# Performance work log

Hardware: AMD Instinct MI355X
Metric: run time of the kernel (lower is better)

## Reference

```python
import jax, jax.numpy as jnp
import numpy as np

EMB_DIM = 1024
NUM_HEAD = 16
HEAD_DIM = EMB_DIM // NUM_HEAD
B, S = 2, 2048


def setup_inputs() -> dict:
    key = jax.random.key(0)
    ks = jax.random.split(key, 10)
    scale = 1.0 / np.sqrt(EMB_DIM)
    x = jax.random.normal(ks[0], (B, S, EMB_DIM), dtype=jnp.float32)
    # causal mask: 1 = keep, 0 = masked out (torch masked_fill(mask == 0, -inf))
    mask = jnp.tril(jnp.ones((S, S), dtype=jnp.int32))[None, None, :, :]
    def lin(kw, kb):
        W = jax.random.uniform(kw, (EMB_DIM, EMB_DIM), jnp.float32, -scale, scale)
        b = jax.random.uniform(kb, (EMB_DIM,), jnp.float32, -scale, scale)
        return W, b
    Wq, bq = lin(ks[1], ks[2])
    Wk, bk = lin(ks[3], ks[4])
    Wv, bv = lin(ks[5], ks[6])
    Wo, bo = lin(ks[7], ks[8])
    return {"x": x, "mask": mask, "Wq": Wq, "bq": bq, "Wk": Wk, "bk": bk,
            "Wv": Wv, "bv": bv, "Wo": Wo, "bo": bo}


def reference(x, mask, Wq, bq, Wk, bk, Wv, bv, Wo, bo):
    Bsz, Sq, _ = x.shape
    # projections; torch Linear: y = x @ W^T + b
    def proj(W, b):
        y = jnp.einsum('bse,fe->bsf', x, W) + b
        return y.reshape(Bsz, Sq, NUM_HEAD, HEAD_DIM).transpose(0, 2, 1, 3)  # [B,H,S,D]
    q = proj(Wq, bq)
    k = proj(Wk, bk)
    v = proj(Wv, bv)
    scaling = jnp.asarray(HEAD_DIM ** 0.5, x.dtype)
    scores = jnp.einsum('bhqd,bhkd->bhqk', q, k) / scaling  # [B,H,S,S]
    scores = jnp.where(mask == 0, -jnp.inf, scores)
    attn = jax.nn.softmax(scores, axis=-1)
    out = jnp.einsum('bhqk,bhkd->bhqd', attn, v)
    out = out.transpose(0, 2, 1, 3).reshape(Bsz, Sq, EMB_DIM)
    return jnp.einsum('bse,fe->bsf', out, Wo) + bo
```

## Files before the change

kernel.cpp:

```cpp
#include <hip/hip_runtime.h>

typedef unsigned short u16;
typedef __attribute__((ext_vector_type(8))) __bf16 bf16x8;
typedef __attribute__((ext_vector_type(8))) short  short8;
typedef __attribute__((ext_vector_type(4))) short  short4v;
typedef __attribute__((ext_vector_type(4))) float  floatx4;

constexpr int Bc = 2, Sc = 2048, Ec = 1024, Hc = 16, Dc = 64;
constexpr int Mc = Bc * Sc;

#define NEG_BIG (-1.0e30f)

__device__ __forceinline__ u16 f2b(float f) {
  union { float f; unsigned u; } c; c.f = f;
  unsigned u = c.u;
  return (u16)((u + 0x7fffu + ((u >> 16) & 1u)) >> 16);
}
__device__ __forceinline__ short8 ld8(const u16* p) { return *(const short8*)p; }

__device__ __forceinline__ floatx4 mfma16(short8 a, short8 b, floatx4 c) {
  return __builtin_amdgcn_mfma_f32_16x16x32_bf16(
      __builtin_bit_cast(bf16x8, a), __builtin_bit_cast(bf16x8, b), c, 0, 0, 0);
}

__device__ __forceinline__ void async16(const u16* g, u16* l) {
  __builtin_amdgcn_global_load_lds(
      (const __attribute__((address_space(1))) void*)g,
      (__attribute__((address_space(3))) void*)l, 16, 0, 0);
}

__global__ __launch_bounds__(256) void cvt_kernel(
    const float* __restrict__ x,  const float* __restrict__ Wq,
    const float* __restrict__ Wk, const float* __restrict__ Wv,
    const float* __restrict__ Wo, u16* __restrict__ dst) {
  const size_t i = ((size_t)blockIdx.x * 256 + threadIdx.x) * 4;
  const int seg = (int)(i >> 20);
  const float* src;
  size_t off;
  if (seg < 4)       { src = x;  off = i; }
  else if (seg == 4) { src = Wq; off = i - ((size_t)4 << 20); }
  else if (seg == 5) { src = Wk; off = i - ((size_t)5 << 20); }
  else if (seg == 6) { src = Wv; off = i - ((size_t)6 << 20); }
  else               { src = Wo; off = i - ((size_t)7 << 20); }
  floatx4 v = *(const floatx4*)(src + off);
  short4v o;
  o[0] = (short)f2b(v[0]); o[1] = (short)f2b(v[1]);
  o[2] = (short)f2b(v[2]); o[3] = (short)f2b(v[3]);
  *(short4v*)(dst + i) = o;
}

__device__ __forceinline__ void gemm128(
    const u16* __restrict__ A, const u16* __restrict__ B, int K,
    int m0, int n0, u16* As, u16* Bs, floatx4 acc[4][4]) {
  const int t = threadIdx.x;
  const int w = t >> 6, lane = t & 63;
  const int wm = w & 1, wn = w >> 1;
  const int quad = lane >> 4, l16 = lane & 15;
  const int r = t >> 2;
  const int c = (t & 3) * 8;

#pragma unroll
  for (int i = 0; i < 4; ++i)
#pragma unroll
    for (int j = 0; j < 4; ++j) acc[i][j] = 0.f;

  for (int k0 = 0; k0 < K; k0 += 32) {
#pragma unroll
    for (int jj = 0; jj < 2; ++jj) {
      async16(A + (size_t)(m0 + jj * 64 + r) * K + k0 + c, As + jj * 2048 + w * 512);
      async16(B + (size_t)(n0 + jj * 64 + r) * K + k0 + c, Bs + jj * 2048 + w * 512);
    }
    __syncthreads();
    short8 af[4], bfr[4];
#pragma unroll
    for (int i = 0; i < 4; ++i)
      af[i]  = *(const short8*)(As + (wm * 64 + i * 16 + l16) * 32 + quad * 8);
#pragma unroll
    for (int j = 0; j < 4; ++j)
      bfr[j] = *(const short8*)(Bs + (wn * 64 + j * 16 + l16) * 32 + quad * 8);
#pragma unroll
    for (int i = 0; i < 4; ++i)
#pragma unroll
      for (int j = 0; j < 4; ++j)
        acc[i][j] = mfma16(af[i], bfr[j], acc[i][j]);
    __syncthreads();
  }
}

__global__ __launch_bounds__(256) void qkv_mm(
    const u16* __restrict__ xb, const u16* __restrict__ Wb,
    const float* __restrict__ bq, const float* __restrict__ bk,
    const float* __restrict__ bv,
    u16* __restrict__ Q, u16* __restrict__ K_, u16* __restrict__ Vt) {
  __shared__ __align__(16) u16 As[4096], Bs[4096];
  const int z = blockIdx.z;
  const u16* W = Wb + ((size_t)z << 20);
  const float* bias = (z == 0) ? bq : (z == 1) ? bk : bv;
  const int m0 = blockIdx.y * 128, n0 = blockIdx.x * 128;

  floatx4 acc[4][4];
  gemm128(xb, W, Ec, m0, n0, As, Bs, acc);

  const int t = threadIdx.x, w = t >> 6, lane = t & 63;
  const int wm = w & 1, wn = w >> 1, quad = lane >> 4, l16 = lane & 15;
#pragma unroll
  for (int i = 0; i < 4; ++i)
#pragma unroll
    for (int j = 0; j < 4; ++j)
#pragma unroll
      for (int rr = 0; rr < 4; ++rr) {
        const int row = m0 + wm * 64 + i * 16 + quad * 4 + rr;
        const int col = n0 + wn * 64 + j * 16 + l16;
        const float v = acc[i][j][rr] + bias[col];
        const int bb = row >> 11, s = row & (Sc - 1);
        const int h = col >> 6, d = col & (Dc - 1), bh = bb * Hc + h;
        if (z < 2) ((z == 0) ? Q : K_)[((size_t)bh * Sc + s) * Dc + d] = f2b(v);
        else       Vt[((size_t)bh * Dc + d) * Sc + s] = f2b(v);
      }
}

__global__ __launch_bounds__(256) void proj_mm(
    const u16* __restrict__ O, const u16* __restrict__ Wob,
    const float* __restrict__ bias, float* __restrict__ out) {
  __shared__ __align__(16) u16 As[4096], Bs[4096];
  const int m0 = blockIdx.y * 128, n0 = blockIdx.x * 128;

  floatx4 acc[4][4];
  gemm128(O, Wob, Ec, m0, n0, As, Bs, acc);

  const int t = threadIdx.x, w = t >> 6, lane = t & 63;
  const int wm = w & 1, wn = w >> 1, quad = lane >> 4, l16 = lane & 15;
#pragma unroll
  for (int i = 0; i < 4; ++i)
#pragma unroll
    for (int j = 0; j < 4; ++j)
#pragma unroll
      for (int rr = 0; rr < 4; ++rr) {
        const int row = m0 + wm * 64 + i * 16 + quad * 4 + rr;
        const int col = n0 + wn * 64 + j * 16 + l16;
        out[(size_t)row * Ec + col] = acc[i][j][rr] + bias[col];
      }
}

__device__ __forceinline__ void attn_stream(
    int q0, const u16* __restrict__ Qh, const u16* __restrict__ Kh,
    const u16* __restrict__ Vh, u16* __restrict__ O, int bb, int h,
    u16* Ks, u16* Vs, u16* Pw) {
  const int t = threadIdx.x;
  const int w = t >> 6, lane = t & 63;
  const int quad = lane >> 4, l16 = lane & 15;

  const int sr = w * 8 + (lane >> 3);
  const int sb = (lane & 7) ^ (lane >> 3);
  const int swz = l16 & 7;

  const u16* qrow_p = Qh + (size_t)(q0 + w * 16 + l16) * Dc;
  const short8 aq0 = ld8(qrow_p + quad * 8);
  const short8 aq1 = ld8(qrow_p + 32 + quad * 8);

  float   mrow[4], lrow[4];
  floatx4 oacc[4];
#pragma unroll
  for (int r = 0; r < 4; ++r) { mrow[r] = NEG_BIG; lrow[r] = 0.f; }
#pragma unroll
  for (int dt = 0; dt < 4; ++dt) oacc[dt] = 0.f;

  for (int kt = 0; kt <= q0; kt += 128) {
#pragma unroll
    for (int st = 0; st < 2; ++st)
#pragma unroll
      for (int it = 0; it < 2; ++it) {
        const int r = it * 32 + sr;
        async16(Kh + (size_t)(kt + st * 64 + r) * Dc + sb * 8,
                Ks + st * 4096 + it * 2048 + w * 512);
        async16(Vh + (size_t)r * Sc + kt + st * 64 + sb * 8,
                Vs + st * 4096 + it * 2048 + w * 512);
      }
    __syncthreads();

    floatx4 sacc[8];
#pragma unroll
    for (int nt = 0; nt < 8; ++nt) sacc[nt] = 0.f;
#pragma unroll
    for (int ks = 0; ks < 2; ++ks) {
      const short8 a = ks ? aq1 : aq0;
#pragma unroll
      for (int nt = 0; nt < 8; ++nt) {
        const short8 b = *(const short8*)(
            Ks + (nt >> 2) * 4096 + ((nt & 3) * 16 + l16) * 64 +
            (((ks * 4 + quad) ^ swz) * 8));
        sacc[nt] = mfma16(a, b, sacc[nt]);
      }
    }

    const bool diag = (kt + 128 > q0);
#pragma unroll
    for (int r = 0; r < 4; ++r) {
      const int qrow = q0 + w * 16 + quad * 4 + r;
      float sv[8];
      float mx = NEG_BIG;
#pragma unroll
      for (int nt = 0; nt < 8; ++nt) {
        float s = sacc[nt][r] * 0.125f;
        const int col = kt + nt * 16 + l16;
        s = (diag && col > qrow) ? NEG_BIG : s;
        sv[nt] = s;
        mx = fmaxf(mx, s);
      }
#pragma unroll
      for (int sh = 1; sh < 16; sh <<= 1) mx = fmaxf(mx, __shfl_xor(mx, sh, 16));
      const float mnew  = fmaxf(mrow[r], mx);
      const float alpha = __expf(mrow[r] - mnew);
      float sum = 0.f;
#pragma unroll
      for (int nt = 0; nt < 8; ++nt) {
        const float pv = __expf(sv[nt] - mnew);
        sv[nt] = pv;
        sum += pv;
      }
#pragma unroll
      for (int sh = 1; sh < 16; sh <<= 1) sum += __shfl_xor(sum, sh, 16);
      lrow[r] = lrow[r] * alpha + sum;
      mrow[r] = mnew;
#pragma unroll
      for (int dt = 0; dt < 4; ++dt) oacc[dt][r] *= alpha;
#pragma unroll
      for (int nt = 0; nt < 8; ++nt)
        Pw[(nt >> 2) * 1216 + (quad * 4 + r) * 76 + (nt & 3) * 16 + l16] =
            f2b(sv[nt]);
    }

#pragma unroll
    for (int kc = 0; kc < 4; ++kc) {
      const short8 a =
          ld8(Pw + (kc >> 1) * 1216 + l16 * 76 + (kc & 1) * 32 + quad * 8);
#pragma unroll
      for (int dt = 0; dt < 4; ++dt) {
        const short8 b = *(const short8*)(
            Vs + (kc >> 1) * 4096 + (dt * 16 + l16) * 64 +
            ((((kc & 1) * 4 + quad) ^ swz) * 8));
        oacc[dt] = mfma16(a, b, oacc[dt]);
      }
    }
    __syncthreads();
  }

#pragma unroll
  for (int dt = 0; dt < 4; ++dt) {
#pragma unroll
    for (int r = 0; r < 4; ++r) {
      const int qrow = q0 + w * 16 + quad * 4 + r;
      const float ov = oacc[dt][r] / lrow[r];
      O[((size_t)(bb * Sc + qrow)) * Ec + h * Dc + dt * 16 + l16] = f2b(ov);
    }
  }
}

__global__ __launch_bounds__(256) void attn_kernel(
    const u16* __restrict__ Q, const u16* __restrict__ K,
    const u16* __restrict__ Vt, u16* __restrict__ O) {
  const int p  = blockIdx.x;
  const int bh = blockIdx.y;
  const int bb = bh >> 4, h = bh & 15;

  const u16* Qh = Q  + (size_t)bh * Sc * Dc;
  const u16* Kh = K  + (size_t)bh * Sc * Dc;
  const u16* Vh = Vt + (size_t)bh * Dc * Sc;

  __shared__ __align__(16) u16 Ks[8192];
  __shared__ __align__(16) u16 Vs[8192];
  __shared__ __align__(16) u16 Pl[4 * 2 * 1216];

  u16* const Pw = Pl + (threadIdx.x >> 6) * 2 * 1216;

  attn_stream((31 - p) * 64, Qh, Kh, Vh, O, bb, h, Ks, Vs, Pw);
  __syncthreads();
  attn_stream(p * 64, Qh, Kh, Vh, O, bb, h, Ks, Vs, Pw);
}

extern "C" void kernel_launch(void* const* d_in, const int* in_sizes, int n_in,
                              void* d_out, int out_size, void* d_ws, size_t ws_size,
                              hipStream_t stream) {
  const float* x  = (const float*)d_in[0];
  const float* Wq = (const float*)d_in[2];
  const float* bq = (const float*)d_in[3];
  const float* Wk = (const float*)d_in[4];
  const float* bk = (const float*)d_in[5];
  const float* Wv = (const float*)d_in[6];
  const float* bv = (const float*)d_in[7];
  const float* Wo = (const float*)d_in[8];
  const float* bo = (const float*)d_in[9];

  const size_t MiE = (size_t)Mc * Ec;
  u16* Q  = (u16*)d_ws;
  u16* K  = Q  + MiE;
  u16* Vt = K  + MiE;
  u16* O  = Vt + MiE;
  u16* xb = O  + MiE;
  u16* Wb = xb + MiE;
  u16* Wob = Wb + ((size_t)3 << 20);

  cvt_kernel<<<8192, 256, 0, stream>>>(x, Wq, Wk, Wv, Wo, xb);
  qkv_mm<<<dim3(Ec / 128, Mc / 128, 3), 256, 0, stream>>>(
      xb, Wb, bq, bk, bv, Q, K, Vt);
  attn_kernel<<<dim3(16, Bc * Hc), 256, 0, stream>>>(Q, K, Vt, O);
  proj_mm<<<dim3(Ec / 128, Mc / 128), 256, 0, stream>>>(O, Wob, bo, (float*)d_out);
}
```

Before: 243.8 us.

## Fold softmax scale into Q, use exp2, shrink P buffer, one q-tile per block

```diff
diff --git a/kernel.cpp b/kernel.cpp
--- a/kernel.cpp
+++ b/kernel.cpp
@@ -10,11 +10,16 @@
 constexpr int Mc = Bc * Sc;
 
 #define NEG_BIG (-1.0e30f)
+#define QSCALE  0.18033688011112042f
 
 __device__ __forceinline__ u16 f2b(float f) {
   union { float f; unsigned u; } c; c.f = f;
   unsigned u = c.u;
   return (u16)((u + 0x7fffu + ((u >> 16) & 1u)) >> 16);
+}
+__device__ __forceinline__ u16 f2b_fast(float f) {
+  union { float f; unsigned u; } c; c.f = f;
+  return (u16)((c.u + 0x8000u) >> 16);
 }
 __device__ __forceinline__ short8 ld8(const u16* p) { return *(const short8*)p; }
 
@@ -111,7 +116,8 @@
       for (int rr = 0; rr < 4; ++rr) {
         const int row = m0 + wm * 64 + i * 16 + quad * 4 + rr;
         const int col = n0 + wn * 64 + j * 16 + l16;
-        const float v = acc[i][j][rr] + bias[col];
+        float v = acc[i][j][rr] + bias[col];
+        if (z == 0) v *= QSCALE;
         const int bb = row >> 11, s = row & (Sc - 1);
         const int h = col >> 6, d = col & (Dc - 1), bh = bb * Hc + h;
         if (z < 2) ((z == 0) ? Q : K_)[((size_t)bh * Sc + s) * Dc + d] = f2b(v);
@@ -142,13 +148,26 @@
       }
 }
 
-__device__ __forceinline__ void attn_stream(
-    int q0, const u16* __restrict__ Qh, const u16* __restrict__ Kh,
-    const u16* __restrict__ Vh, u16* __restrict__ O, int bb, int h,
-    u16* Ks, u16* Vs, u16* Pw) {
+__global__ __launch_bounds__(256, 4) void attn_kernel(
+    const u16* __restrict__ Q, const u16* __restrict__ K,
+    const u16* __restrict__ Vt, u16* __restrict__ O) {
+  const int qt = 31 - (int)((blockIdx.x + blockIdx.y) & 31);
+  const int q0 = qt * 64;
+  const int bh = blockIdx.y;
+  const int bb = bh >> 4, h = bh & 15;
+
+  const u16* Qh = Q  + (size_t)bh * Sc * Dc;
+  const u16* Kh = K  + (size_t)bh * Sc * Dc;
+  const u16* Vh = Vt + (size_t)bh * Dc * Sc;
+
   const int t = threadIdx.x;
   const int w = t >> 6, lane = t & 63;
   const int quad = lane >> 4, l16 = lane & 15;
+
+  __shared__ __align__(16) u16 Ks[8192];
+  __shared__ __align__(16) u16 Vs[8192];
+  __shared__ __align__(16) u16 Pl[4096];
+  u16* const Pw = Pl + w * 1024;
 
   const int sr = w * 8 + (lane >> 3);
   const int sb = (lane & 7) ^ (lane >> 3);
@@ -194,27 +213,30 @@
     }
 
     const bool diag = (kt + 128 > q0);
+    float s2buf[4][4];
 #pragma unroll
     for (int r = 0; r < 4; ++r) {
-      const int qrow = q0 + w * 16 + quad * 4 + r;
+      const int row = quad * 4 + r;
       float sv[8];
+#pragma unroll
+      for (int nt = 0; nt < 8; ++nt) sv[nt] = sacc[nt][r];
+      if (diag) {
+        const int qrow = q0 + w * 16 + row;
+#pragma unroll
+        for (int nt = 0; nt < 8; ++nt)
+          if (kt + nt * 16 + l16 > qrow) sv[nt] = NEG_BIG;
+      }
       float mx = NEG_BIG;
 #pragma unroll
-      for (int nt = 0; nt < 8; ++nt) {
-        float s = sacc[nt][r] * 0.125f;
-        const int col = kt + nt * 16 + l16;
-        s = (diag && col > qrow) ? NEG_BIG : s;
-        sv[nt] = s;
-        mx = fmaxf(mx, s);
-      }
+      for (int nt = 0; nt < 8; ++nt) mx = fmaxf(mx, sv[nt]);
 #pragma unroll
       for (int sh = 1; sh < 16; sh <<= 1) mx = fmaxf(mx, __shfl_xor(mx, sh, 16));
       const float mnew  = fmaxf(mrow[r], mx);
-      const float alpha = __expf(mrow[r] - mnew);
+      const float alpha = exp2f(mrow[r] - mnew);
       float sum = 0.f;
 #pragma unroll
       for (int nt = 0; nt < 8; ++nt) {
-        const float pv = __expf(sv[nt] - mnew);
+        const float pv = exp2f(sv[nt] - mnew);
         sv[nt] = pv;
         sum += pv;
       }
@@ -224,21 +246,42 @@
       mrow[r] = mnew;
 #pragma unroll
       for (int dt = 0; dt < 4; ++dt) oacc[dt][r] *= alpha;
-#pragma unroll
-      for (int nt = 0; nt < 8; ++nt)
-        Pw[(nt >> 2) * 1216 + (quad * 4 + r) * 76 + (nt & 3) * 16 + l16] =
-            f2b(sv[nt]);
-    }
-
-#pragma unroll
-    for (int kc = 0; kc < 4; ++kc) {
-      const short8 a =
-          ld8(Pw + (kc >> 1) * 1216 + l16 * 76 + (kc & 1) * 32 + quad * 8);
+      const int sx = row & 7;
+#pragma unroll
+      for (int j = 0; j < 4; ++j) {
+        Pw[row * 64 + (((2 * j + (l16 >> 3)) ^ sx) * 8) + (l16 & 7)] =
+            f2b_fast(sv[j]);
+        s2buf[r][j] = sv[4 + j];
+      }
+    }
+
+#pragma unroll
+    for (int kc = 0; kc < 2; ++kc) {
+      const short8 a = ld8(Pw + l16 * 64 + (((kc * 4 + quad) ^ swz) * 8));
 #pragma unroll
       for (int dt = 0; dt < 4; ++dt) {
         const short8 b = *(const short8*)(
-            Vs + (kc >> 1) * 4096 + (dt * 16 + l16) * 64 +
-            ((((kc & 1) * 4 + quad) ^ swz) * 8));
+            Vs + (dt * 16 + l16) * 64 + (((kc * 4 + quad) ^ swz) * 8));
+        oacc[dt] = mfma16(a, b, oacc[dt]);
+      }
+    }
+
+#pragma unroll
+    for (int r = 0; r < 4; ++r) {
+      const int row = quad * 4 + r, sx = row & 7;
+#pragma unroll
+      for (int j = 0; j < 4; ++j)
+        Pw[row * 64 + (((2 * j + (l16 >> 3)) ^ sx) * 8) + (l16 & 7)] =
+            f2b_fast(s2buf[r][j]);
+    }
+
+#pragma unroll
+    for (int kc = 0; kc < 2; ++kc) {
+      const short8 a = ld8(Pw + l16 * 64 + (((kc * 4 + quad) ^ swz) * 8));
+#pragma unroll
+      for (int dt = 0; dt < 4; ++dt) {
+        const short8 b = *(const short8*)(
+            Vs + 4096 + (dt * 16 + l16) * 64 + (((kc * 4 + quad) ^ swz) * 8));
         oacc[dt] = mfma16(a, b, oacc[dt]);
       }
     }
@@ -254,28 +297,6 @@
       O[((size_t)(bb * Sc + qrow)) * Ec + h * Dc + dt * 16 + l16] = f2b(ov);
     }
   }
-}
-
-__global__ __launch_bounds__(256) void attn_kernel(
-    const u16* __restrict__ Q, const u16* __restrict__ K,
-    const u16* __restrict__ Vt, u16* __restrict__ O) {
-  const int p  = blockIdx.x;
-  const int bh = blockIdx.y;
-  const int bb = bh >> 4, h = bh & 15;
-
-  const u16* Qh = Q  + (size_t)bh * Sc * Dc;
-  const u16* Kh = K  + (size_t)bh * Sc * Dc;
-  const u16* Vh = Vt + (size_t)bh * Dc * Sc;
-
-  __shared__ __align__(16) u16 Ks[8192];
-  __shared__ __align__(16) u16 Vs[8192];
-  __shared__ __align__(16) u16 Pl[4 * 2 * 1216];
-
-  u16* const Pw = Pl + (threadIdx.x >> 6) * 2 * 1216;
-
-  attn_stream((31 - p) * 64, Qh, Kh, Vh, O, bb, h, Ks, Vs, Pw);
-  __syncthreads();
-  attn_stream(p * 64, Qh, Kh, Vh, O, bb, h, Ks, Vs, Pw);
 }
 
 extern "C" void kernel_launch(void* const* d_in, const int* in_sizes, int n_in,
@@ -303,6 +324,6 @@
   cvt_kernel<<<8192, 256, 0, stream>>>(x, Wq, Wk, Wv, Wo, xb);
   qkv_mm<<<dim3(Ec / 128, Mc / 128, 3), 256, 0, stream>>>(
       xb, Wb, bq, bk, bv, Q, K, Vt);
-  attn_kernel<<<dim3(16, Bc * Hc), 256, 0, stream>>>(Q, K, Vt, O);
+  attn_kernel<<<dim3(32, Bc * Hc), 256, 0, stream>>>(Q, K, Vt, O);
   proj_mm<<<dim3(Ec / 128, Mc / 128), 256, 0, stream>>>(O, Wob, bo, (float*)d_out);
 }
```

Result: faster. 234.9 us (-3.6%).
